# Kernel tuning notes

Hardware: AMD Instinct MI355X
Metric: run time of the kernel (lower is better)

## Reference

```python
import jax, jax.numpy as jnp
import numpy as np

B, CIN, COUT, H, W = 32, 2048, 1024, 32, 32  # requires COUT == H*W


def setup_inputs() -> dict:
    key = jax.random.key(0)
    ks = jax.random.split(key, 7)
    s_in = 1.0 / np.sqrt(CIN)
    s_out = 1.0 / np.sqrt(COUT)
    return {
        "x": jax.random.normal(ks[0], (B, CIN, H, W), dtype=jnp.float32),
        "w_reduce": jax.random.uniform(ks[1], (COUT, CIN), jnp.float32, -s_in, s_in),
        "b_reduce": jax.random.uniform(ks[2], (COUT,), jnp.float32, -s_in, s_in),
        "w_collect": jax.random.uniform(ks[3], (COUT, COUT), jnp.float32, -s_out, s_out),
        "b_collect": jax.random.uniform(ks[4], (COUT,), jnp.float32, -s_out, s_out),
        "w_distribute": jax.random.uniform(ks[5], (COUT, COUT), jnp.float32, -s_out, s_out),
        "b_distribute": jax.random.uniform(ks[6], (COUT,), jnp.float32, -s_out, s_out),
    }


def _conv1x1(x, w, b):
    # x: [b, c_in, h, w], w: [c_out, c_in] -> [b, c_out, h, w]
    return jnp.einsum('bchw,oc->bohw', x, w) + b[None, :, None, None]


def reference(x, w_reduce, b_reduce, w_collect, b_collect, w_distribute, b_distribute):
    x = _conv1x1(x, w_reduce, b_reduce)           # [b, c, h, w]
    b, c, h, w = x.shape
    hw = h * w
    x_collect = _conv1x1(x, w_collect, b_collect).reshape(b, c, hw)
    x_collect = jax.nn.softmax(x_collect, axis=-1)            # softmax over hw
    x_distribute = _conv1x1(x, w_distribute, b_distribute).reshape(b, c, hw)
    x_distribute = jax.nn.softmax(x_distribute, axis=1)       # softmax over c
    # bmm: [b,c,hw] @ [b,hw,c] -> [b,c,c]; valid reshape since c == hw
    x_att = jnp.einsum('bcn,bdn->bcd', x_collect, x_distribute).reshape(b, c, h, w)
    return x + x_att
```

## Files before the change

### kernel.cpp

```cpp
#include <hip/hip_runtime.h>
#include <stdint.h>

typedef __attribute__((ext_vector_type(8))) short short8;
typedef __attribute__((ext_vector_type(4))) float floatx4;

#define GLOAD_LDS16(gp, lp)                                        \
  __builtin_amdgcn_global_load_lds(                                \
      (const __attribute__((address_space(1))) void*)(gp),         \
      (__attribute__((address_space(3))) void*)(lp), 16, 0, 0)

__device__ __forceinline__ float bf2f(unsigned short u) {
  union { unsigned int i; float f; } x;
  x.i = ((unsigned int)u) << 16;
  return x.f;
}
__device__ __forceinline__ unsigned short f2bf(float f) {
  union { float f; unsigned int i; } x;
  x.f = f;
  unsigned int r = x.i + 0x7FFFu + ((x.i >> 16) & 1u);
  return (unsigned short)(r >> 16);
}

template <int EPI>
__launch_bounds__(256, 2)
__global__ void gemm_abt(const unsigned short* __restrict__ A, long strideA,
                         const unsigned short* __restrict__ Bt, long strideB,
                         const float* __restrict__ bias,
                         const float* addSrc, void* outP,
                         long strideOut, int N, int K)
{
  __shared__ short Asm[128 * 64];
  __shared__ short Bsm[128 * 64];

  const int tid  = threadIdx.x;
  const int wave = tid >> 6;
  const int lane = tid & 63;
  const int z  = blockIdx.z;
  const int m0 = blockIdx.y * 128;
  const int n0 = blockIdx.x * 128;

  const unsigned short* Ab = A  + (size_t)z * strideA;
  const unsigned short* Bb = Bt + (size_t)z * strideB;

  const int lr  = lane >> 3;
  const int swz = (lane & 7) ^ lr;
  const unsigned short* gA = Ab + (size_t)(m0 + wave * 32 + lr) * K + swz * 8;
  const unsigned short* gB = Bb + (size_t)(n0 + wave * 32 + lr) * K + swz * 8;
  short* lA = Asm + wave * 32 * 64;
  short* lB = Bsm + wave * 32 * 64;

  floatx4 acc[4][4];
#pragma unroll
  for (int i = 0; i < 4; ++i)
#pragma unroll
    for (int j = 0; j < 4; ++j)
#pragma unroll
      for (int q = 0; q < 4; ++q) acc[i][j][q] = 0.f;

  const int g    = lane >> 4;
  const int ln16 = lane & 15;
  const int wr   = (wave >> 1) * 64;
  const int wc   = (wave & 1) * 64;
  const int xm   = (lane & 7) * 8;
  const int ck0  = (g * 8) ^ xm;
  const int ck1  = (32 + g * 8) ^ xm;

  const int nkt = K >> 6;
  for (int kt = 0; kt < nkt; ++kt) {
#pragma unroll
    for (int i = 0; i < 4; ++i) {
      GLOAD_LDS16(gA + (size_t)i * 8 * K, lA + i * 512);
      GLOAD_LDS16(gB + (size_t)i * 8 * K, lB + i * 512);
    }
    __syncthreads();
#pragma unroll
    for (int kk = 0; kk < 2; ++kk) {
      const int ck = kk ? ck1 : ck0;
      short8 a[4], b[4];
#pragma unroll
      for (int m = 0; m < 4; ++m)
        a[m] = *(const short8*)(Asm + (wr + m * 16 + ln16) * 64 + ck);
#pragma unroll
      for (int n = 0; n < 4; ++n)
        b[n] = *(const short8*)(Bsm + (wc + n * 16 + ln16) * 64 + ck);
#pragma unroll
      for (int m = 0; m < 4; ++m)
#pragma unroll
        for (int n = 0; n < 4; ++n)
          acc[m][n] = __builtin_amdgcn_mfma_f32_16x16x32_bf16(a[m], b[n], acc[m][n], 0, 0, 0);
    }
    __syncthreads();
    gA += 64;
    gB += 64;
  }

#pragma unroll
  for (int m = 0; m < 4; ++m) {
#pragma unroll
    for (int q = 0; q < 4; ++q) {
      const int row = m0 + wr + m * 16 + g * 4 + q;
      float bv = 0.f;
      if constexpr (EPI != 2) bv = bias[row];
#pragma unroll
      for (int n = 0; n < 4; ++n) {
        const int col = n0 + wc + n * 16 + ln16;
        const size_t idx = (size_t)z * strideOut + (size_t)row * N + col;
        const float v = acc[m][n][q] + bv;
        if constexpr (EPI == 0) {
          ((float*)outP)[idx] = v;
        } else if constexpr (EPI == 1) {
          ((unsigned short*)outP)[idx] = f2bf(v);
        } else {
          ((float*)outP)[idx] = v + addSrc[idx];
        }
      }
    }
  }
}

__launch_bounds__(256)
__global__ void transpose_f32_bf16(const float* __restrict__ src,
                                   unsigned short* __restrict__ dst,
                                   int R, int C, long sB, long dB)
{
  __shared__ float tile[32][33];
  const int z  = blockIdx.z;
  const int r0 = blockIdx.y * 32;
  const int c0 = blockIdx.x * 32;
  const float* s = src + (size_t)z * sB;
  unsigned short* d = dst + (size_t)z * dB;
  const int tx = threadIdx.x;
  const int ty = threadIdx.y;
#pragma unroll
  for (int k = 0; k < 4; ++k)
    tile[ty + 8 * k][tx] = s[(size_t)(r0 + ty + 8 * k) * C + (c0 + tx)];
  __syncthreads();
#pragma unroll
  for (int k = 0; k < 4; ++k)
    d[(size_t)(c0 + ty + 8 * k) * R + (r0 + tx)] = f2bf(tile[tx][ty + 8 * k]);
}

__launch_bounds__(256)
__global__ void convert_f32_bf16(const float* __restrict__ s,
                                 unsigned short* __restrict__ d, int n4)
{
  const int i = blockIdx.x * 256 + threadIdx.x;
  if (i >= n4) return;
  const float4 f = ((const float4*)s)[i];
  ushort4 o;
  o.x = f2bf(f.x); o.y = f2bf(f.y); o.z = f2bf(f.z); o.w = f2bf(f.w);
  ((ushort4*)d)[i] = o;
}

__launch_bounds__(256)
__global__ void softmax_row(unsigned short* __restrict__ data, long batchStride)
{
  const int z = blockIdx.y;
  unsigned short* row = data + (size_t)z * batchStride + (size_t)blockIdx.x * 1024;
  const int t = threadIdx.x;
  const int wave = t >> 6, lane = t & 63;
  const ushort4 u = ((const ushort4*)row)[t];
  const float v0 = bf2f(u.x), v1 = bf2f(u.y), v2 = bf2f(u.z), v3 = bf2f(u.w);
  float m = fmaxf(fmaxf(v0, v1), fmaxf(v2, v3));
#pragma unroll
  for (int off = 32; off > 0; off >>= 1) m = fmaxf(m, __shfl_xor(m, off));
  __shared__ float rm[4], rs[4];
  if (lane == 0) rm[wave] = m;
  __syncthreads();
  m = fmaxf(fmaxf(rm[0], rm[1]), fmaxf(rm[2], rm[3]));
  const float e0 = __expf(v0 - m), e1 = __expf(v1 - m);
  const float e2 = __expf(v2 - m), e3 = __expf(v3 - m);
  float s = e0 + e1 + e2 + e3;
#pragma unroll
  for (int off = 32; off > 0; off >>= 1) s += __shfl_xor(s, off);
  if (lane == 0) rs[wave] = s;
  __syncthreads();
  const float inv = 1.f / (rs[0] + rs[1] + rs[2] + rs[3]);
  ushort4 o;
  o.x = f2bf(e0 * inv); o.y = f2bf(e1 * inv);
  o.z = f2bf(e2 * inv); o.w = f2bf(e3 * inv);
  ((ushort4*)row)[t] = o;
}

__launch_bounds__(256)
__global__ void softmax_col(unsigned short* __restrict__ data, long batchStride,
                            long baseOff)
{
  const int z = blockIdx.y;
  unsigned short* D = data + (size_t)z * batchStride + baseOff;
  const int jl  = threadIdx.x & 63;
  const int j   = blockIdx.x * 64 + jl;
  const int rs0 = threadIdx.x >> 6;
  float m = -3.0e38f, s = 0.f;
  for (int r = rs0; r < 1024; r += 4) {
    const float v = bf2f(D[(size_t)r * 1024 + j]);
    const float nm = fmaxf(m, v);
    s = s * __expf(m - nm) + __expf(v - nm);
    m = nm;
  }
  __shared__ float sm[4][64], ss[4][64], fm[64], fs[64];
  sm[rs0][jl] = m;
  ss[rs0][jl] = s;
  __syncthreads();
  if (threadIdx.x < 64) {
    const float M = fmaxf(fmaxf(sm[0][jl], sm[1][jl]), fmaxf(sm[2][jl], sm[3][jl]));
    const float S = ss[0][jl] * __expf(sm[0][jl] - M) + ss[1][jl] * __expf(sm[1][jl] - M) +
                    ss[2][jl] * __expf(sm[2][jl] - M) + ss[3][jl] * __expf(sm[3][jl] - M);
    fm[jl] = M;
    fs[jl] = 1.f / S;
  }
  __syncthreads();
  const float M = fm[jl], inv = fs[jl];
  for (int r = rs0; r < 1024; r += 4) {
    const size_t idx = (size_t)r * 1024 + j;
    D[idx] = f2bf(__expf(bf2f(D[idx]) - M) * inv);
  }
}

extern "C" void kernel_launch(void* const* d_in, const int* in_sizes, int n_in,
                              void* d_out, int out_size, void* d_ws, size_t ws_size,
                              hipStream_t stream)
{
  (void)in_sizes; (void)n_in; (void)out_size; (void)ws_size;
  const float* x  = (const float*)d_in[0];
  const float* wr = (const float*)d_in[1];
  const float* br = (const float*)d_in[2];
  const float* wc = (const float*)d_in[3];
  const float* bc = (const float*)d_in[4];
  const float* wd = (const float*)d_in[5];
  const float* bd = (const float*)d_in[6];

  const size_t MiB = 1024 * 1024;
  char* ws = (char*)d_ws;
  unsigned short* xT   = (unsigned short*)ws;
  unsigned short* Lout = (unsigned short*)ws;
  unsigned short* YT   = (unsigned short*)(ws + 128 * MiB);
  unsigned short* wrB  = (unsigned short*)(ws + 192 * MiB);
  unsigned short* wcdB = (unsigned short*)(ws + 196 * MiB);
  float*          bcd  = (float*)(ws + 200 * MiB);
  float*          Yf   = (float*)d_out;

  convert_f32_bf16<<<2048, 256, 0, stream>>>(wr, wrB, 524288);
  convert_f32_bf16<<<1024, 256, 0, stream>>>(wc, wcdB, 262144);
  convert_f32_bf16<<<1024, 256, 0, stream>>>(wd, wcdB + 1048576, 262144);
  hipMemcpyAsync(bcd,        bc, 1024 * sizeof(float), hipMemcpyDeviceToDevice, stream);
  hipMemcpyAsync(bcd + 1024, bd, 1024 * sizeof(float), hipMemcpyDeviceToDevice, stream);

  transpose_f32_bf16<<<dim3(32, 64, 32), dim3(32, 8), 0, stream>>>(
      x, xT, 2048, 1024, (long)2048 * 1024, (long)1024 * 2048);

  gemm_abt<0><<<dim3(8, 8, 32), 256, 0, stream>>>(
      wrB, 0L, xT, (long)1024 * 2048, br, nullptr, (void*)Yf,
      (long)1024 * 1024, 1024, 2048);

  transpose_f32_bf16<<<dim3(32, 32, 32), dim3(32, 8), 0, stream>>>(
      Yf, YT, 1024, 1024, (long)1024 * 1024, (long)1024 * 1024);

  gemm_abt<1><<<dim3(8, 16, 32), 256, 0, stream>>>(
      wcdB, 0L, YT, (long)1024 * 1024, bcd, nullptr, (void*)Lout,
      (long)2048 * 1024, 1024, 1024);

  softmax_row<<<dim3(1024, 32), 256, 0, stream>>>(Lout, (long)2048 * 1024);
  softmax_col<<<dim3(16, 32), 256, 0, stream>>>(Lout, (long)2048 * 1024, (long)1024 * 1024);

  gemm_abt<2><<<dim3(8, 8, 32), 256, 0, stream>>>(
      Lout, (long)2048 * 1024, Lout + (size_t)1024 * 1024, (long)2048 * 1024,
      nullptr, Yf, (void*)d_out, (long)1024 * 1024, 1024, 1024);
}
```

Before: 1.108 ms.

## Swizzle GEMM block order across XCDs, vectorize transposes and column softmax

The GEMM grid is flattened to 1D and remapped so that consecutive block IDs landing on the same XCD cover neighbouring tiles of the same batch, which should improve L2 reuse. The transpose kernel now uses 64x64 tiles with float4 loads and 16-byte bf16 stores. The column softmax is rewritten to use 16-byte row loads with 8 columns per thread and separate max, sum and normalize passes with a shared-memory tree reduction. The extra read pass in the softmax and the remap index arithmetic add some cost, offset by wider memory accesses.

```diff
diff --git a/kernel.cpp b/kernel.cpp
--- a/kernel.cpp
+++ b/kernel.cpp
@@ -27,25 +27,32 @@
                          const unsigned short* __restrict__ Bt, long strideB,
                          const float* __restrict__ bias,
                          const float* addSrc, void* outP,
-                         long strideOut, int N, int K)
+                         long strideOut, int N, int K, int nbx, int nby)
 {
   __shared__ short Asm[128 * 64];
   __shared__ short Bsm[128 * 64];
+
+  const int nwg = gridDim.x;
+  const int bid = blockIdx.x;
+  const int q   = nwg >> 3;
+  const int swz = (bid & 7) * q + (bid >> 3);
+  const int bx  = swz % nbx;
+  const int by  = (swz / nbx) % nby;
+  const int z   = swz / (nbx * nby);
 
   const int tid  = threadIdx.x;
   const int wave = tid >> 6;
   const int lane = tid & 63;
-  const int z  = blockIdx.z;
-  const int m0 = blockIdx.y * 128;
-  const int n0 = blockIdx.x * 128;
+  const int m0 = by * 128;
+  const int n0 = bx * 128;
 
   const unsigned short* Ab = A  + (size_t)z * strideA;
   const unsigned short* Bb = Bt + (size_t)z * strideB;
 
   const int lr  = lane >> 3;
-  const int swz = (lane & 7) ^ lr;
-  const unsigned short* gA = Ab + (size_t)(m0 + wave * 32 + lr) * K + swz * 8;
-  const unsigned short* gB = Bb + (size_t)(n0 + wave * 32 + lr) * K + swz * 8;
+  const int swzc = (lane & 7) ^ lr;
+  const unsigned short* gA = Ab + (size_t)(m0 + wave * 32 + lr) * K + swzc * 8;
+  const unsigned short* gB = Bb + (size_t)(n0 + wave * 32 + lr) * K + swzc * 8;
   short* lA = Asm + wave * 32 * 64;
   short* lB = Bsm + wave * 32 * 64;
 
@@ -55,7 +62,7 @@
 #pragma unroll
     for (int j = 0; j < 4; ++j)
 #pragma unroll
-      for (int q = 0; q < 4; ++q) acc[i][j][q] = 0.f;
+      for (int p = 0; p < 4; ++p) acc[i][j][p] = 0.f;
 
   const int g    = lane >> 4;
   const int ln16 = lane & 15;
@@ -97,15 +104,15 @@
 #pragma unroll
   for (int m = 0; m < 4; ++m) {
 #pragma unroll
-    for (int q = 0; q < 4; ++q) {
-      const int row = m0 + wr + m * 16 + g * 4 + q;
+    for (int p = 0; p < 4; ++p) {
+      const int row = m0 + wr + m * 16 + g * 4 + p;
       float bv = 0.f;
       if constexpr (EPI != 2) bv = bias[row];
 #pragma unroll
       for (int n = 0; n < 4; ++n) {
         const int col = n0 + wc + n * 16 + ln16;
         const size_t idx = (size_t)z * strideOut + (size_t)row * N + col;
-        const float v = acc[m][n][q] + bv;
+        const float v = acc[m][n][p] + bv;
         if constexpr (EPI == 0) {
           ((float*)outP)[idx] = v;
         } else if constexpr (EPI == 1) {
@@ -123,21 +130,35 @@
                                    unsigned short* __restrict__ dst,
                                    int R, int C, long sB, long dB)
 {
-  __shared__ float tile[32][33];
+  __shared__ float tile[64][65];
   const int z  = blockIdx.z;
-  const int r0 = blockIdx.y * 32;
-  const int c0 = blockIdx.x * 32;
+  const int r0 = blockIdx.y * 64;
+  const int c0 = blockIdx.x * 64;
   const float* s = src + (size_t)z * sB;
   unsigned short* d = dst + (size_t)z * dB;
-  const int tx = threadIdx.x;
-  const int ty = threadIdx.y;
-#pragma unroll
-  for (int k = 0; k < 4; ++k)
-    tile[ty + 8 * k][tx] = s[(size_t)(r0 + ty + 8 * k) * C + (c0 + tx)];
-  __syncthreads();
-#pragma unroll
-  for (int k = 0; k < 4; ++k)
-    d[(size_t)(c0 + ty + 8 * k) * R + (r0 + tx)] = f2bf(tile[tx][ty + 8 * k]);
+  const int t  = threadIdx.x;
+  const int tx = t & 15;
+  const int ty = t >> 4;
+#pragma unroll
+  for (int k = 0; k < 4; ++k) {
+    const int row = ty + 16 * k;
+    const float4 v = *(const float4*)(s + (size_t)(r0 + row) * C + (c0 + 4 * tx));
+    tile[row][4 * tx + 0] = v.x;
+    tile[row][4 * tx + 1] = v.y;
+    tile[row][4 * tx + 2] = v.z;
+    tile[row][4 * tx + 3] = v.w;
+  }
+  __syncthreads();
+  const int cc = t >> 3;
+  const int rc = t & 7;
+#pragma unroll
+  for (int k = 0; k < 2; ++k) {
+    const int c = cc + 32 * k;
+    short8 o;
+#pragma unroll
+    for (int j = 0; j < 8; ++j) o[j] = (short)f2bf(tile[8 * rc + j][c]);
+    *(short8*)(d + (size_t)(c0 + c) * R + (r0 + 8 * rc)) = o;
+  }
 }
 
 __launch_bounds__(256)
@@ -186,34 +207,70 @@
 __global__ void softmax_col(unsigned short* __restrict__ data, long batchStride,
                             long baseOff)
 {
+  __shared__ float red[32][64];
   const int z = blockIdx.y;
-  unsigned short* D = data + (size_t)z * batchStride + baseOff;
-  const int jl  = threadIdx.x & 63;
-  const int j   = blockIdx.x * 64 + jl;
-  const int rs0 = threadIdx.x >> 6;
-  float m = -3.0e38f, s = 0.f;
-  for (int r = rs0; r < 1024; r += 4) {
-    const float v = bf2f(D[(size_t)r * 1024 + j]);
-    const float nm = fmaxf(m, v);
-    s = s * __expf(m - nm) + __expf(v - nm);
-    m = nm;
-  }
-  __shared__ float sm[4][64], ss[4][64], fm[64], fs[64];
-  sm[rs0][jl] = m;
-  ss[rs0][jl] = s;
-  __syncthreads();
-  if (threadIdx.x < 64) {
-    const float M = fmaxf(fmaxf(sm[0][jl], sm[1][jl]), fmaxf(sm[2][jl], sm[3][jl]));
-    const float S = ss[0][jl] * __expf(sm[0][jl] - M) + ss[1][jl] * __expf(sm[1][jl] - M) +
-                    ss[2][jl] * __expf(sm[2][jl] - M) + ss[3][jl] * __expf(sm[3][jl] - M);
-    fm[jl] = M;
-    fs[jl] = 1.f / S;
-  }
-  __syncthreads();
-  const float M = fm[jl], inv = fs[jl];
-  for (int r = rs0; r < 1024; r += 4) {
-    const size_t idx = (size_t)r * 1024 + j;
-    D[idx] = f2bf(__expf(bf2f(D[idx]) - M) * inv);
+  unsigned short* D = data + (size_t)z * batchStride + baseOff + blockIdx.x * 64;
+  const int tx = threadIdx.x & 7;
+  const int ty = threadIdx.x >> 3;
+  const int cb = tx * 8;
+
+  float M[8];
+#pragma unroll
+  for (int j = 0; j < 8; ++j) M[j] = -3.0e38f;
+#pragma unroll 4
+  for (int r = ty; r < 1024; r += 32) {
+    const short8 v = *(const short8*)(D + (size_t)r * 1024 + cb);
+#pragma unroll
+    for (int j = 0; j < 8; ++j) M[j] = fmaxf(M[j], bf2f((unsigned short)v[j]));
+  }
+#pragma unroll
+  for (int j = 0; j < 8; ++j) red[ty][cb + j] = M[j];
+  for (int h = 16; h >= 1; h >>= 1) {
+    __syncthreads();
+    if (ty < h) {
+#pragma unroll
+      for (int j = 0; j < 8; ++j)
+        red[ty][cb + j] = fmaxf(red[ty][cb + j], red[ty + h][cb + j]);
+    }
+  }
+  __syncthreads();
+#pragma unroll
+  for (int j = 0; j < 8; ++j) M[j] = red[0][cb + j];
+  __syncthreads();
+
+  float S[8];
+#pragma unroll
+  for (int j = 0; j < 8; ++j) S[j] = 0.f;
+#pragma unroll 4
+  for (int r = ty; r < 1024; r += 32) {
+    const short8 v = *(const short8*)(D + (size_t)r * 1024 + cb);
+#pragma unroll
+    for (int j = 0; j < 8; ++j) S[j] += __expf(bf2f((unsigned short)v[j]) - M[j]);
+  }
+#pragma unroll
+  for (int j = 0; j < 8; ++j) red[ty][cb + j] = S[j];
+  for (int h = 16; h >= 1; h >>= 1) {
+    __syncthreads();
+    if (ty < h) {
+#pragma unroll
+      for (int j = 0; j < 8; ++j)
+        red[ty][cb + j] += red[ty + h][cb + j];
+    }
+  }
+  __syncthreads();
+  float I[8];
+#pragma unroll
+  for (int j = 0; j < 8; ++j) I[j] = 1.f / red[0][cb + j];
+
+#pragma unroll 2
+  for (int r = ty; r < 1024; r += 32) {
+    const size_t off = (size_t)r * 1024 + cb;
+    const short8 v = *(const short8*)(D + off);
+    short8 o;
+#pragma unroll
+    for (int j = 0; j < 8; ++j)
+      o[j] = (short)f2bf(__expf(bf2f((unsigned short)v[j]) - M[j]) * I[j]);
+    *(short8*)(D + off) = o;
   }
 }
 
@@ -246,24 +303,24 @@
   hipMemcpyAsync(bcd,        bc, 1024 * sizeof(float), hipMemcpyDeviceToDevice, stream);
   hipMemcpyAsync(bcd + 1024, bd, 1024 * sizeof(float), hipMemcpyDeviceToDevice, stream);
 
-  transpose_f32_bf16<<<dim3(32, 64, 32), dim3(32, 8), 0, stream>>>(
+  transpose_f32_bf16<<<dim3(16, 32, 32), 256, 0, stream>>>(
       x, xT, 2048, 1024, (long)2048 * 1024, (long)1024 * 2048);
 
-  gemm_abt<0><<<dim3(8, 8, 32), 256, 0, stream>>>(
+  gemm_abt<0><<<2048, 256, 0, stream>>>(
       wrB, 0L, xT, (long)1024 * 2048, br, nullptr, (void*)Yf,
-      (long)1024 * 1024, 1024, 2048);
-
-  transpose_f32_bf16<<<dim3(32, 32, 32), dim3(32, 8), 0, stream>>>(
+      (long)1024 * 1024, 1024, 2048, 8, 8);
+
+  transpose_f32_bf16<<<dim3(16, 16, 32), 256, 0, stream>>>(
       Yf, YT, 1024, 1024, (long)1024 * 1024, (long)1024 * 1024);
 
-  gemm_abt<1><<<dim3(8, 16, 32), 256, 0, stream>>>(
+  gemm_abt<1><<<4096, 256, 0, stream>>>(
       wcdB, 0L, YT, (long)1024 * 1024, bcd, nullptr, (void*)Lout,
-      (long)2048 * 1024, 1024, 1024);
+      (long)2048 * 1024, 1024, 1024, 8, 16);
 
   softmax_row<<<dim3(1024, 32), 256, 0, stream>>>(Lout, (long)2048 * 1024);
   softmax_col<<<dim3(16, 32), 256, 0, stream>>>(Lout, (long)2048 * 1024, (long)1024 * 1024);
 
-  gemm_abt<2><<<dim3(8, 8, 32), 256, 0, stream>>>(
+  gemm_abt<2><<<2048, 256, 0, stream>>>(
       Lout, (long)2048 * 1024, Lout + (size_t)1024 * 1024, (long)2048 * 1024,
-      nullptr, Yf, (void*)d_out, (long)1024 * 1024, 1024, 1024);
-}
+      nullptr, Yf, (void*)d_out, (long)1024 * 1024, 1024, 1024, 8, 8);
+}
```

Result: faster. 973.7 us (-12.1%).
